# Kernel optimization log

Measured on AMD Instinct MI355X. Metric: run time of the kernel, lower is better.

## Reference

```python
import jax, jax.numpy as jnp
import numpy as np


def _aggregate(x, w, k, pad):
    """Involution-style per-pixel local conv.
    x: [N, C, H, W]; w: [N, heads, wc, k*k, H, W] (stride=1, dilation=1, zero pad).
    Returns [N, heads, C, H, W].
    """
    N, C, H, W = x.shape
    heads, wc = w.shape[1], w.shape[2]
    G = C // wc  # channel groups sharing the same per-pixel weights (c % wc)
    xp = jnp.pad(x, ((0, 0), (0, 0), (pad, pad), (pad, pad)))
    # unfold: [N, C, k*k, H, W] via k*k static shifted slices (no dynamic indexing)
    patches = jnp.stack(
        [xp[:, :, i:i + H, j:j + W] for i in range(k) for j in range(k)], axis=2
    )
    p = patches.reshape(N, G, wc, k * k, H, W)
    # out[n, e, g, v, h, w] = sum_k w[n, e, v, k, h, w] * p[n, g, v, k, h, w]
    out = jnp.einsum('nevkhw,ngvkhw->negvhw', w, p)
    return out.reshape(N, heads, C, H, W)


def reference(x, weight1, weight2):
    out1 = _aggregate(x, weight1, 3, 1)  # 3x3 branch, pad=1
    out2 = _aggregate(x, weight2, 5, 2)  # 5x5 branch, pad=2
    # output layout [N, 2, heads, C, H, W] matching the CUDA index arithmetic
    return jnp.stack([out1, out2], axis=1)


def setup_inputs() -> dict:
    key = jax.random.key(0)
    k1, k2, k3 = jax.random.split(key, 3)
    N, C, H, W = 4, 256, 56, 56
    heads, wc = 1, 32
    x = jax.random.normal(k1, (N, C, H, W), dtype=jnp.float32)
    weight1 = jax.random.normal(k2, (N, heads, wc, 9, H, W), dtype=jnp.float32)
    weight2 = jax.random.normal(k3, (N, heads, wc, 25, H, W), dtype=jnp.float32)
    return {"x": x, "weight1": weight1, "weight2": weight2}
```

## Files before the change

kernel.cpp:

```cpp
#include <hip/hip_runtime.h>


#define N_  4
#define C_  256
#define H_  56
#define W_  56
#define HW_ 3136
#define WC_ 32

#define LROWS   12
#define LSTRIDE 64

__global__ __launch_bounds__(256) void lconv_kernel(
    const float* __restrict__ x,
    const float* __restrict__ w1,
    const float* __restrict__ w2,
    float* __restrict__ out)
{
    __shared__ float lds[4 * LROWS * LSTRIDE];

    const int b    = blockIdx.x;
    const int tile = b % 7;
    const int gsel = (b / 7) & 1;
    const int v    = (b / 14) & 31;
    const int n    = b / 448;
    const int r0   = tile * 8;
    const int nv   = n * WC_ + v;
    const int tid  = threadIdx.x;

    for (int idx = tid; idx < 672; idx += 256) {
        const int c4 = idx % 14;
        const int t2 = idx / 14;
        const int lr = t2 % LROWS;
        const int pl = t2 / LROWS;
        const int gr = r0 - 2 + lr;
        float4 val = make_float4(0.f, 0.f, 0.f, 0.f);
        if (gr >= 0 && gr < H_) {
            const int ch = gsel * 128 + pl * 32 + v;
            val = *(const float4*)(x + (size_t)(n * C_ + ch) * HW_ + gr * W_ + c4 * 4);
        }
        *(float4*)&lds[(pl * LROWS + lr) * LSTRIDE + 4 + c4 * 4] = val;
    }
    if (tid < 192) {
        const int pl = tid / 48;
        const int lr = (tid % 48) / 4;
        const int k  = tid & 3;
        const int slot = (k < 2) ? (2 + k) : (58 + k);
        lds[(pl * LROWS + lr) * LSTRIDE + slot] = 0.f;
    }
    __syncthreads();

    const int row = tid >> 5;
    const int cp  = tid & 31;
    if (cp >= 28) return;

    const int h  = r0 + row;
    const int wb = cp * 2;
    const int hw = h * W_ + wb;

    const float* w1t = w1 + (size_t)nv * 9  * HW_ + hw;
    const float* w2t = w2 + (size_t)nv * 25 * HW_ + hw;

    float a1x[4] = {0.f,0.f,0.f,0.f}, a1y[4] = {0.f,0.f,0.f,0.f};
    float a2x[4] = {0.f,0.f,0.f,0.f}, a2y[4] = {0.f,0.f,0.f,0.f};

    #pragma unroll 1
    for (int di = 0; di < 5; ++di) {
        const bool inner = (di >= 1) && (di <= 3);

        float2 wr2[5];
        #pragma unroll
        for (int dj = 0; dj < 5; ++dj)
            wr2[dj] = *(const float2*)(w2t + (size_t)(di * 5 + dj) * HW_);
        float2 wr1[3] = {make_float2(0.f,0.f), make_float2(0.f,0.f), make_float2(0.f,0.f)};
        if (inner) {
            #pragma unroll
            for (int dj = 0; dj < 3; ++dj)
                wr1[dj] = *(const float2*)(w1t + (size_t)((di - 1) * 3 + dj) * HW_);
        }

        float2 xwa[4], xwb[4], xwc[4];
        #pragma unroll
        for (int j = 0; j < 4; ++j) {
            const float* lp = &lds[(j * LROWS + row + di) * LSTRIDE + wb + 2];
            xwa[j] = *(const float2*)(lp);
            xwb[j] = *(const float2*)(lp + 2);
            xwc[j] = *(const float2*)(lp + 4);
        }

        #pragma unroll
        for (int j = 0; j < 4; ++j) {
            const float xw[6] = {xwa[j].x, xwa[j].y, xwb[j].x, xwb[j].y, xwc[j].x, xwc[j].y};
            #pragma unroll
            for (int dj = 0; dj < 5; ++dj) {
                a2x[j] += wr2[dj].x * xw[dj];
                a2y[j] += wr2[dj].y * xw[dj + 1];
            }
            if (inner) {
                #pragma unroll
                for (int dj = 0; dj < 3; ++dj) {
                    a1x[j] += wr1[dj].x * xw[dj + 1];
                    a1y[j] += wr1[dj].y * xw[dj + 2];
                }
            }
        }
    }

    const int c0 = gsel * 128 + v;
    float* o1 = out + ((size_t)(n * 2 + 0) * C_ + c0) * HW_ + hw;
    float* o2 = out + ((size_t)(n * 2 + 1) * C_ + c0) * HW_ + hw;
    #pragma unroll
    for (int j = 0; j < 4; ++j) {
        *(float2*)(o1 + (size_t)j * WC_ * HW_) = make_float2(a1x[j], a1y[j]);
        *(float2*)(o2 + (size_t)j * WC_ * HW_) = make_float2(a2x[j], a2y[j]);
    }
}

extern "C" void kernel_launch(void* const* d_in, const int* in_sizes, int n_in,
                              void* d_out, int out_size, void* d_ws, size_t ws_size,
                              hipStream_t stream) {
    const float* x  = (const float*)d_in[0];
    const float* w1 = (const float*)d_in[1];
    const float* w2 = (const float*)d_in[2];
    float* out = (float*)d_out;

    dim3 grid(4 * 32 * 2 * 7), block(256);
    hipLaunchKernelGGL(lconv_kernel, grid, block, 0, stream, x, w1, w2, out);
}
```

Before: 112.8 us.

## Widen per-thread work to four pixels and enlarge row tiles to fourteen

Each thread now computes four adjacent output pixels with float4 weight loads, LDS reads and stores, instead of two pixels with float2 accesses. Tiles grow from 8 to 14 rows, so there are 1024 blocks instead of 1792 and less halo reload per block. The LDS padding layout is shifted so the 8-wide input windows stay aligned. In exchange, only 196 of 256 threads compute, more registers are used, and the grid is smaller, which may reduce occupancy and latency hiding.

```diff
diff --git a/kernel.cpp b/kernel.cpp
--- a/kernel.cpp
+++ b/kernel.cpp
@@ -8,7 +8,8 @@
 #define HW_ 3136
 #define WC_ 32
 
-#define LROWS   12
+#define TILE    14
+#define LROWS   18
 #define LSTRIDE 64
 
 __global__ __launch_bounds__(256) void lconv_kernel(
@@ -20,15 +21,15 @@
     __shared__ float lds[4 * LROWS * LSTRIDE];
 
     const int b    = blockIdx.x;
-    const int tile = b % 7;
-    const int gsel = (b / 7) & 1;
-    const int v    = (b / 14) & 31;
-    const int n    = b / 448;
-    const int r0   = tile * 8;
+    const int tile = b & 3;
+    const int gsel = (b >> 2) & 1;
+    const int v    = (b >> 3) & 31;
+    const int n    = b >> 8;
+    const int r0   = tile * TILE;
     const int nv   = n * WC_ + v;
     const int tid  = threadIdx.x;
 
-    for (int idx = tid; idx < 672; idx += 256) {
+    for (int idx = tid; idx < 4 * LROWS * 14; idx += 256) {
         const int c4 = idx % 14;
         const int t2 = idx / 14;
         const int lr = t2 % LROWS;
@@ -39,69 +40,78 @@
             const int ch = gsel * 128 + pl * 32 + v;
             val = *(const float4*)(x + (size_t)(n * C_ + ch) * HW_ + gr * W_ + c4 * 4);
         }
-        *(float4*)&lds[(pl * LROWS + lr) * LSTRIDE + 4 + c4 * 4] = val;
+        float* lp = &lds[(pl * LROWS + lr) * LSTRIDE + 4 * c4 + 2];
+        *(float2*)(lp)     = make_float2(val.x, val.y);
+        *(float2*)(lp + 2) = make_float2(val.z, val.w);
     }
-    if (tid < 192) {
-        const int pl = tid / 48;
-        const int lr = (tid % 48) / 4;
-        const int k  = tid & 3;
-        const int slot = (k < 2) ? (2 + k) : (58 + k);
+    for (int idx = tid; idx < 4 * LROWS * 4; idx += 256) {
+        const int k  = idx & 3;
+        const int t2 = idx >> 2;
+        const int lr = t2 % LROWS;
+        const int pl = t2 / LROWS;
+        const int slot = (k < 2) ? k : (56 + k);
         lds[(pl * LROWS + lr) * LSTRIDE + slot] = 0.f;
     }
     __syncthreads();
 
-    const int row = tid >> 5;
-    const int cp  = tid & 31;
-    if (cp >= 28) return;
+    if (tid >= TILE * 14) return;
 
-    const int h  = r0 + row;
-    const int wb = cp * 2;
-    const int hw = h * W_ + wb;
+    const int row = tid / 14;
+    const int s   = tid % 14;
+    const int wb  = 4 * s;
+    const int h   = r0 + row;
+    const int hw  = h * W_ + wb;
 
     const float* w1t = w1 + (size_t)nv * 9  * HW_ + hw;
     const float* w2t = w2 + (size_t)nv * 25 * HW_ + hw;
 
-    float a1x[4] = {0.f,0.f,0.f,0.f}, a1y[4] = {0.f,0.f,0.f,0.f};
-    float a2x[4] = {0.f,0.f,0.f,0.f}, a2y[4] = {0.f,0.f,0.f,0.f};
+    float a1[4][4], a2[4][4];
+    #pragma unroll
+    for (int g = 0; g < 4; ++g)
+        #pragma unroll
+        for (int p = 0; p < 4; ++p) { a1[g][p] = 0.f; a2[g][p] = 0.f; }
 
     #pragma unroll 1
     for (int di = 0; di < 5; ++di) {
         const bool inner = (di >= 1) && (di <= 3);
 
-        float2 wr2[5];
+        float wr2[5][4];
         #pragma unroll
-        for (int dj = 0; dj < 5; ++dj)
-            wr2[dj] = *(const float2*)(w2t + (size_t)(di * 5 + dj) * HW_);
-        float2 wr1[3] = {make_float2(0.f,0.f), make_float2(0.f,0.f), make_float2(0.f,0.f)};
+        for (int dj = 0; dj < 5; ++dj) {
+            const float4 t = *(const float4*)(w2t + (size_t)(di * 5 + dj) * HW_);
+            wr2[dj][0] = t.x; wr2[dj][1] = t.y; wr2[dj][2] = t.z; wr2[dj][3] = t.w;
+        }
+        float wr1[3][4];
+        #pragma unroll
+        for (int dj = 0; dj < 3; ++dj)
+            #pragma unroll
+            for (int p = 0; p < 4; ++p) wr1[dj][p] = 0.f;
         if (inner) {
             #pragma unroll
-            for (int dj = 0; dj < 3; ++dj)
-                wr1[dj] = *(const float2*)(w1t + (size_t)((di - 1) * 3 + dj) * HW_);
-        }
-
-        float2 xwa[4], xwb[4], xwc[4];
-        #pragma unroll
-        for (int j = 0; j < 4; ++j) {
-            const float* lp = &lds[(j * LROWS + row + di) * LSTRIDE + wb + 2];
-            xwa[j] = *(const float2*)(lp);
-            xwb[j] = *(const float2*)(lp + 2);
-            xwc[j] = *(const float2*)(lp + 4);
+            for (int dj = 0; dj < 3; ++dj) {
+                const float4 t = *(const float4*)(w1t + (size_t)((di - 1) * 3 + dj) * HW_);
+                wr1[dj][0] = t.x; wr1[dj][1] = t.y; wr1[dj][2] = t.z; wr1[dj][3] = t.w;
+            }
         }
 
         #pragma unroll
-        for (int j = 0; j < 4; ++j) {
-            const float xw[6] = {xwa[j].x, xwa[j].y, xwb[j].x, xwb[j].y, xwc[j].x, xwc[j].y};
+        for (int g = 0; g < 4; ++g) {
+            const float* lp = &lds[(g * LROWS + row + di) * LSTRIDE + wb];
+            const float4 xa = *(const float4*)(lp);
+            const float4 xb4 = *(const float4*)(lp + 4);
+            const float xw[8] = {xa.x, xa.y, xa.z, xa.w, xb4.x, xb4.y, xb4.z, xb4.w};
+
             #pragma unroll
-            for (int dj = 0; dj < 5; ++dj) {
-                a2x[j] += wr2[dj].x * xw[dj];
-                a2y[j] += wr2[dj].y * xw[dj + 1];
-            }
+            for (int dj = 0; dj < 5; ++dj)
+                #pragma unroll
+                for (int p = 0; p < 4; ++p)
+                    a2[g][p] += wr2[dj][p] * xw[p + dj];
             if (inner) {
                 #pragma unroll
-                for (int dj = 0; dj < 3; ++dj) {
-                    a1x[j] += wr1[dj].x * xw[dj + 1];
-                    a1y[j] += wr1[dj].y * xw[dj + 2];
-                }
+                for (int dj = 0; dj < 3; ++dj)
+                    #pragma unroll
+                    for (int p = 0; p < 4; ++p)
+                        a1[g][p] += wr1[dj][p] * xw[p + dj + 1];
             }
         }
     }
@@ -110,9 +120,11 @@
     float* o1 = out + ((size_t)(n * 2 + 0) * C_ + c0) * HW_ + hw;
     float* o2 = out + ((size_t)(n * 2 + 1) * C_ + c0) * HW_ + hw;
     #pragma unroll
-    for (int j = 0; j < 4; ++j) {
-        *(float2*)(o1 + (size_t)j * WC_ * HW_) = make_float2(a1x[j], a1y[j]);
-        *(float2*)(o2 + (size_t)j * WC_ * HW_) = make_float2(a2x[j], a2y[j]);
+    for (int g = 0; g < 4; ++g) {
+        *(float4*)(o1 + (size_t)g * WC_ * HW_) =
+            make_float4(a1[g][0], a1[g][1], a1[g][2], a1[g][3]);
+        *(float4*)(o2 + (size_t)g * WC_ * HW_) =
+            make_float4(a2[g][0], a2[g][1], a2[g][2], a2[g][3]);
     }
 }
 
@@ -124,6 +136,6 @@
     const float* w2 = (const float*)d_in[2];
     float* out = (float*)d_out;
 
-    dim3 grid(4 * 32 * 2 * 7), block(256);
+    dim3 grid(4 * 2 * 32 * 4), block(256);
     hipLaunchKernelGGL(lconv_kernel, grid, block, 0, stream, x, w1, w2, out);
 }
```

New measurement: 114.2 us. No clear change (+1.3%).
